# Kernel optimization log

Hardware: AMD Instinct MI355X
Metric: run time of the kernel (lower is better)

The kernel has to match this reference:

```python
import jax, jax.numpy as jnp
import numpy as np

IN_SIZE = 1024
HID = 2048
OUT = 1024
M_STEPS = 100   # max extra ponder steps -> up to M_STEPS+1 total steps
EPS = 0.01


def setup_inputs() -> dict:
    key = jax.random.key(0)
    ks = jax.random.split(key, 11)
    inv = 1.0 / np.sqrt(HID)

    def unif(k, shape, scale):
        return jax.random.uniform(k, shape, jnp.float32, -scale, scale)

    return {
        "x": jax.random.normal(ks[0], (IN_SIZE,), jnp.float32),
        "h0": jax.random.normal(ks[1], (HID,), jnp.float32) * 0.1,
        "c0": jax.random.normal(ks[2], (HID,), jnp.float32) * 0.1,
        "W_ih": unif(ks[3], (4 * HID, 1 + IN_SIZE), inv),
        "b_ih": unif(ks[4], (4 * HID,), inv),
        "W_hh": unif(ks[5], (4 * HID, HID), inv),
        "b_hh": unif(ks[6], (4 * HID,), inv),
        "w_halt": unif(ks[7], (HID,), inv),
        "b_halt": jnp.ones((1,), jnp.float32),  # fc_halt.bias = 1.0 per source
        "W_out": unif(ks[8], (OUT, HID), inv),
        "b_out": unif(ks[9], (OUT,), inv),
    }


def reference(x, h0, c0, W_ih, b_ih, W_hh, b_hh, w_halt, b_halt, W_out, b_out):
    # Input contribution is constant across steps except the prepended halt flag
    # (1 on first step, 0 after). Precompute it once.
    ih_x = W_ih[:, 1:] @ x + b_ih + b_hh      # (4H,)
    w_flag = W_ih[:, 0]                        # (4H,)

    def step(carry, flag):
        h, c = carry
        gates = ih_x + flag * w_flag + W_hh @ h  # (4H,)
        i, f, g, o = jnp.split(gates, 4)
        i = jax.nn.sigmoid(i)
        f = jax.nn.sigmoid(f)
        g = jnp.tanh(g)
        o = jax.nn.sigmoid(o)
        c = f * c + i * g
        h = o * jnp.tanh(c)
        return (h, c), (h, c)

    flags = jnp.concatenate(
        [jnp.ones((1,), x.dtype), jnp.zeros((M_STEPS,), x.dtype)])
    _, (H, C) = jax.lax.scan(step, (h0, c0), flags)  # (M+1, HID) each

    p = jax.nn.sigmoid(H @ w_halt + b_halt[0])       # (M+1,) halting probs
    csum = jnp.cumsum(p)
    halted = csum >= 1.0 - EPS
    # n = first step where cumulative halt prob crosses threshold, capped at M
    n = jnp.where(jnp.any(halted), jnp.argmax(halted), M_STEPS)
    # remainder r = 1 - sum(p[:n]); csum[n] - p[n] == sum(p[:n])
    r = 1.0 - jnp.where(n > 0, csum[n] - p[n], 0.0)

    idx = jnp.arange(M_STEPS + 1)
    w = jnp.where(idx < n, p, jnp.where(idx == n, r, 0.0))  # (M+1,)

    outputs = H @ W_out.T + b_out                    # (M+1, OUT)
    output = w @ outputs                             # (OUT,) weights sum to 1
    h_out = w @ H                                    # (HID,)
    c_out = w @ C                                    # (HID,)
    ponder = n.astype(x.dtype) + 1.0 + r
    return output, (h_out, c_out), ponder
```

## Files before the change

### kernel.cpp

```cpp
#include <hip/hip_runtime.h>


#define HID    2048
#define INS    1024
#define OUTS   1024
#define MSTEPS 100
#define NBLK   256
#define NTHR   512
#define NWAVE  8
#define JPB    8
#define RPB    32

typedef unsigned long long u64;

__device__ __forceinline__ float wave_reduce(float v) {
    #pragma unroll
    for (int off = 32; off > 0; off >>= 1)
        v += __shfl_down(v, off, 64);
    return v;
}

__device__ __forceinline__ u64 pack_tag(unsigned tag, float v) {
    return ((u64)tag << 32) | (u64)__float_as_uint(v);
}
__device__ __forceinline__ u64 aload(const u64* p) {
    return __hip_atomic_load(p, __ATOMIC_RELAXED, __HIP_MEMORY_SCOPE_AGENT);
}
__device__ __forceinline__ void astore(u64* p, u64 v) {
    __hip_atomic_store(p, v, __ATOMIC_RELAXED, __HIP_MEMORY_SCOPE_AGENT);
}


__global__ __launch_bounds__(NTHR) void alstm_kernel(
    const float* __restrict__ x,      const float* __restrict__ h0,
    const float* __restrict__ c0,     const float* __restrict__ W_ih,
    const float* __restrict__ b_ih,   const float* __restrict__ W_hh,
    const float* __restrict__ b_hh,   const float* __restrict__ w_halt,
    const float* __restrict__ b_halt, const float* __restrict__ W_out,
    const float* __restrict__ b_out,  float* __restrict__ out,
    float* __restrict__ ws)
{
    const int b    = blockIdx.x;
    const int tid  = threadIdx.x;
    const int wave = tid >> 6;
    const int lane = tid & 63;

    float* arrive = ws;
    float* mail   = ws + 1024;
    float* hbuf0  = ws + 2048;
    float* hbuf1  = ws + 2048 + HID;
    float* hbar_g = ws + 2048 + 2 * HID;

    __shared__ float h_lds[HID];
    __shared__ float x_lds[INS];
    __shared__ float gate_lds[RPB];
    __shared__ float ihx_lds[RPB];
    __shared__ float wflag_lds[RPB];
    __shared__ float red_lds[4];
    __shared__ float bcast_lds;
    __shared__ float psum[NWAVE];

    const float bh = b_halt[0];
    const int j_own = b * JPB + tid;

    const int lr0 = 4 * wave;

    #define SYNC_ROUND(tag_, part_, dot_) do {                                 \
        if (tid == 0) {                                                        \
            __threadfence();           \
            astore((u64*)(arrive + 4 * b), pack_tag((tag_), (part_)));         \
        }                                                                      \
        if (b == 0) {                                                          \
            float pf = 0.f;                                                    \
            if (tid < NBLK) {                                                  \
                u64 v;                                                         \
                do { v = aload((u64*)(arrive + 4 * tid)); }                    \
                while ((unsigned)(v >> 32) != (unsigned)(tag_));               \
                pf = __uint_as_float((unsigned)v);                             \
            }                                                                  \
            float s = wave_reduce(pf);                                         \
            if (lane == 0 && wave < 4) red_lds[wave] = s;                      \
            __syncthreads();                                                   \
            if (tid == 0)                                                      \
                bcast_lds = red_lds[0] + red_lds[1] + red_lds[2] + red_lds[3]; \
            __syncthreads();                                                   \
            if (tid < NBLK)                                                    \
                astore((u64*)(mail + 4 * tid), pack_tag((tag_), bcast_lds));   \
        }                                                                      \
        if (tid == 0) {                                                        \
            u64 v;                                                             \
            do { v = aload((u64*)(mail + 4 * b)); }                            \
            while ((unsigned)(v >> 32) != (unsigned)(tag_));                   \
            bcast_lds = __uint_as_float((unsigned)v);                          \
            __threadfence();        \
        }                                                                      \
        __syncthreads();                                                       \
        (dot_) = bcast_lds;                                                    \
    } while (0)

    ((float2*)x_lds)[tid] = ((const float2*)x)[tid];
    ((float4*)h_lds)[tid] = ((const float4*)h0)[tid];
    __syncthreads();

    #pragma unroll
    for (int rr = 0; rr < 4; ++rr) {
        const int lr = lr0 + rr;
        const int r  = (lr >> 3) * HID + b * JPB + (lr & 7);
        const float* wrow = W_ih + (size_t)r * (INS + 1) + 1;
        const int mis = (r + 1) & 3;
        const int p0  = (4 - mis) & 3;
        const int nv  = (INS - p0) >> 2;
        const float4* wv = (const float4*)(wrow + p0);
        float acc = 0.f;
        for (int i = lane; i < nv; i += 64) {
            float4 w4 = wv[i];
            int k = p0 + 4 * i;
            acc += w4.x * x_lds[k] + w4.y * x_lds[k + 1]
                 + w4.z * x_lds[k + 2] + w4.w * x_lds[k + 3];
        }
        if (lane == 0) {
            for (int k = 0; k < p0; ++k)            acc += wrow[k] * x_lds[k];
            for (int k = p0 + 4 * nv; k < INS; ++k) acc += wrow[k] * x_lds[k];
        }
        acc = wave_reduce(acc);
        if (lane == 0) {
            ihx_lds[lr]   = acc + b_ih[r] + b_hh[r];
            wflag_lds[lr] = W_ih[(size_t)r * (INS + 1)];
        }
    }

    float c_reg = 0.f, h_reg = 0.f, hbar = 0.f, cbar = 0.f;
    if (tid < JPB) c_reg = c0[j_own];

    const float4* wr0;
    const float4* wr1;
    const float4* wr2;
    const float4* wr3;
    {
        const int r = (lr0 >> 3) * HID + b * JPB + (lr0 & 7);
        wr0 = (const float4*)(W_hh + (size_t)r * HID);
        wr1 = (const float4*)(W_hh + (size_t)(r + 1) * HID);
        wr2 = (const float4*)(W_hh + (size_t)(r + 2) * HID);
        wr3 = (const float4*)(W_hh + (size_t)(r + 3) * HID);
    }

    float csum = 0.f, r_halt = 0.f;
    int   n_halt = 0;
    for (int t = 0; t <= MSTEPS; ++t) {
        {
            const float4* hv = (const float4*)h_lds;
            float a0 = 0.f, a1 = 0.f, a2 = 0.f, a3 = 0.f;
            #pragma unroll
            for (int m = 0; m < 8; ++m) {
                float4 hh = hv[lane + 64 * m];
                float4 w0 = wr0[lane + 64 * m];
                float4 w1 = wr1[lane + 64 * m];
                float4 w2 = wr2[lane + 64 * m];
                float4 w3 = wr3[lane + 64 * m];
                a0 += w0.x * hh.x + w0.y * hh.y + w0.z * hh.z + w0.w * hh.w;
                a1 += w1.x * hh.x + w1.y * hh.y + w1.z * hh.z + w1.w * hh.w;
                a2 += w2.x * hh.x + w2.y * hh.y + w2.z * hh.z + w2.w * hh.w;
                a3 += w3.x * hh.x + w3.y * hh.y + w3.z * hh.z + w3.w * hh.w;
            }
            a0 = wave_reduce(a0);
            a1 = wave_reduce(a1);
            a2 = wave_reduce(a2);
            a3 = wave_reduce(a3);
            if (lane == 0) {
                #pragma unroll
                for (int rr = 0; rr < 4; ++rr) {
                    float av = (rr == 0) ? a0 : (rr == 1) ? a1 : (rr == 2) ? a2 : a3;
                    float bb = ihx_lds[lr0 + rr];
                    if (t == 0) bb += wflag_lds[lr0 + rr];
                    gate_lds[lr0 + rr] = bb + av;
                }
            }
        }
        __syncthreads();

        float part = 0.f;
        float* hdst = (t & 1) ? hbuf1 : hbuf0;
        if (tid < JPB) {
            float iv = gate_lds[0 * JPB + tid];
            float fv = gate_lds[1 * JPB + tid];
            float gv = gate_lds[2 * JPB + tid];
            float ov = gate_lds[3 * JPB + tid];
            iv = 1.f / (1.f + expf(-iv));
            fv = 1.f / (1.f + expf(-fv));
            gv = tanhf(gv);
            ov = 1.f / (1.f + expf(-ov));
            c_reg = fv * c_reg + iv * gv;
            h_reg = ov * tanhf(c_reg);
            hdst[j_own] = h_reg;
            part = h_reg * w_halt[j_own];
        }
        part += __shfl_down(part, 4, 64);
        part += __shfl_down(part, 2, 64);
        part += __shfl_down(part, 1, 64);

        float dotv;
        SYNC_ROUND(t + 1, part, dotv);

        float p = 1.f / (1.f + expf(-(dotv + bh)));
        float prev = csum;
        csum += p;
        bool halt_now = (csum >= 1.f - 0.01f) || (t == MSTEPS);
        float wt = halt_now ? (1.f - prev) : p;
        if (tid < JPB) { hbar += wt * h_reg; cbar += wt * c_reg; }
        if (halt_now) { n_halt = t; r_halt = 1.f - prev; break; }

        __syncthreads();
        ((float4*)h_lds)[tid] = ((const float4*)hdst)[tid];
        __syncthreads();
    }

    if (tid < JPB) {
        out[OUTS + j_own]       = hbar;
        out[OUTS + HID + j_own] = cbar;
        hbar_g[j_own] = hbar;
    }
    if (b == 0 && tid == 0) out[OUTS + 2 * HID] = (float)(n_halt + 1) + r_halt;

    float dummy;
    SYNC_ROUND(n_halt + 2, 0.f, dummy);
    (void)dummy;

    __syncthreads();
    ((float4*)h_lds)[tid] = ((const float4*)hbar_g)[tid];
    __syncthreads();

    {
        const int row  = b * 4 + (wave & 3);
        const int half = wave >> 2;
        const float4* wrow = (const float4*)(W_out + (size_t)row * HID) + half * 256;
        const float4* hv   = (const float4*)h_lds + half * 256;
        float acc = 0.f;
        #pragma unroll
        for (int m = 0; m < 4; ++m) {
            float4 w4 = wrow[lane + 64 * m];
            float4 h4 = hv[lane + 64 * m];
            acc += w4.x * h4.x + w4.y * h4.y + w4.z * h4.z + w4.w * h4.w;
        }
        acc = wave_reduce(acc);
        if (lane == 0) psum[wave] = acc;
    }
    __syncthreads();
    if (tid < 4) {
        int row = b * 4 + tid;
        out[row] = psum[tid] + psum[tid + 4] + b_out[row];
    }
    #undef SYNC_ROUND
}

extern "C" void kernel_launch(void* const* d_in, const int* in_sizes, int n_in,
                              void* d_out, int out_size, void* d_ws, size_t ws_size,
                              hipStream_t stream) {
    const float* x      = (const float*)d_in[0];
    const float* h0     = (const float*)d_in[1];
    const float* c0     = (const float*)d_in[2];
    const float* W_ih   = (const float*)d_in[3];
    const float* b_ih   = (const float*)d_in[4];
    const float* W_hh   = (const float*)d_in[5];
    const float* b_hh   = (const float*)d_in[6];
    const float* w_halt = (const float*)d_in[7];
    const float* b_halt = (const float*)d_in[8];
    const float* W_out  = (const float*)d_in[9];
    const float* b_out  = (const float*)d_in[10];
    float* out = (float*)d_out;
    float* ws  = (float*)d_ws;

    hipMemsetAsync(d_ws, 0, 8192, stream);

    alstm_kernel<<<dim3(NBLK), dim3(NTHR), 0, stream>>>(
        x, h0, c0, W_ih, b_ih, W_hh, b_hh, w_halt, b_halt, W_out, b_out,
        out, ws);
}
```

Baseline: 187.6 us.

## Keep recurrent and output weight slices resident in registers across all steps

Each wave's four W_hh rows (32 float4 per lane) and its W_out slice (4 float4) are loaded once before the recurrence and held in VGPRs. Empty asm constraints stop the compiler from rematerialising them as reloads. This removes the per-step global/L2 reads of the 32 MB W_hh matrix over the 101 sequential steps. The cost is about 144 extra VGPRs per lane, which risks spilling or lower occupancy, though the persistent grid runs only one 512-thread block per CU.

Result: faster. 177.6 us (-5.3%).

```diff
diff --git a/kernel.cpp b/kernel.cpp
--- a/kernel.cpp
+++ b/kernel.cpp
@@ -12,6 +12,8 @@
 #define RPB    32
 
 typedef unsigned long long u64;
+
+#define KEEP4(v) asm volatile("" : "+v"((v).x), "+v"((v).y), "+v"((v).z), "+v"((v).w))
 
 __device__ __forceinline__ float wave_reduce(float v) {
     #pragma unroll
@@ -64,6 +66,7 @@
     const int j_own = b * JPB + tid;
 
     const int lr0 = 4 * wave;
+    const int rbase = (lr0 >> 3) * HID + b * JPB + (lr0 & 7);
 
     #define SYNC_ROUND(tag_, part_, dot_) do {                                 \
         if (tid == 0) {                                                        \
@@ -98,6 +101,29 @@
         (dot_) = bcast_lds;                                                    \
     } while (0)
 
+    float4 w0r[8], w1r[8], w2r[8], w3r[8];
+    {
+        const float4* p0 = (const float4*)(W_hh + (size_t)rbase * HID);
+        const float4* p1 = (const float4*)(W_hh + (size_t)(rbase + 1) * HID);
+        const float4* p2 = (const float4*)(W_hh + (size_t)(rbase + 2) * HID);
+        const float4* p3 = (const float4*)(W_hh + (size_t)(rbase + 3) * HID);
+        #pragma unroll
+        for (int m = 0; m < 8; ++m) {
+            w0r[m] = p0[lane + 64 * m];
+            w1r[m] = p1[lane + 64 * m];
+            w2r[m] = p2[lane + 64 * m];
+            w3r[m] = p3[lane + 64 * m];
+        }
+    }
+    const int orow  = b * 4 + (wave & 3);
+    const int ohalf = wave >> 2;
+    float4 wor[4];
+    {
+        const float4* po = (const float4*)(W_out + (size_t)orow * HID) + ohalf * 256;
+        #pragma unroll
+        for (int m = 0; m < 4; ++m) wor[m] = po[lane + 64 * m];
+    }
+
     ((float2*)x_lds)[tid] = ((const float2*)x)[tid];
     ((float4*)h_lds)[tid] = ((const float4*)h0)[tid];
     __syncthreads();
@@ -129,20 +155,15 @@
         }
     }
 
+    #pragma unroll
+    for (int m = 0; m < 8; ++m) {
+        KEEP4(w0r[m]); KEEP4(w1r[m]); KEEP4(w2r[m]); KEEP4(w3r[m]);
+    }
+    #pragma unroll
+    for (int m = 0; m < 4; ++m) KEEP4(wor[m]);
+
     float c_reg = 0.f, h_reg = 0.f, hbar = 0.f, cbar = 0.f;
     if (tid < JPB) c_reg = c0[j_own];
-
-    const float4* wr0;
-    const float4* wr1;
-    const float4* wr2;
-    const float4* wr3;
-    {
-        const int r = (lr0 >> 3) * HID + b * JPB + (lr0 & 7);
-        wr0 = (const float4*)(W_hh + (size_t)r * HID);
-        wr1 = (const float4*)(W_hh + (size_t)(r + 1) * HID);
-        wr2 = (const float4*)(W_hh + (size_t)(r + 2) * HID);
-        wr3 = (const float4*)(W_hh + (size_t)(r + 3) * HID);
-    }
 
     float csum = 0.f, r_halt = 0.f;
     int   n_halt = 0;
@@ -153,27 +174,26 @@
             #pragma unroll
             for (int m = 0; m < 8; ++m) {
                 float4 hh = hv[lane + 64 * m];
-                float4 w0 = wr0[lane + 64 * m];
-                float4 w1 = wr1[lane + 64 * m];
-                float4 w2 = wr2[lane + 64 * m];
-                float4 w3 = wr3[lane + 64 * m];
-                a0 += w0.x * hh.x + w0.y * hh.y + w0.z * hh.z + w0.w * hh.w;
-                a1 += w1.x * hh.x + w1.y * hh.y + w1.z * hh.z + w1.w * hh.w;
-                a2 += w2.x * hh.x + w2.y * hh.y + w2.z * hh.z + w2.w * hh.w;
-                a3 += w3.x * hh.x + w3.y * hh.y + w3.z * hh.z + w3.w * hh.w;
+                a0 += w0r[m].x * hh.x + w0r[m].y * hh.y + w0r[m].z * hh.z + w0r[m].w * hh.w;
+                a1 += w1r[m].x * hh.x + w1r[m].y * hh.y + w1r[m].z * hh.z + w1r[m].w * hh.w;
+                a2 += w2r[m].x * hh.x + w2r[m].y * hh.y + w2r[m].z * hh.z + w2r[m].w * hh.w;
+                a3 += w3r[m].x * hh.x + w3r[m].y * hh.y + w3r[m].z * hh.z + w3r[m].w * hh.w;
             }
             a0 = wave_reduce(a0);
             a1 = wave_reduce(a1);
             a2 = wave_reduce(a2);
             a3 = wave_reduce(a3);
             if (lane == 0) {
-                #pragma unroll
-                for (int rr = 0; rr < 4; ++rr) {
-                    float av = (rr == 0) ? a0 : (rr == 1) ? a1 : (rr == 2) ? a2 : a3;
-                    float bb = ihx_lds[lr0 + rr];
-                    if (t == 0) bb += wflag_lds[lr0 + rr];
-                    gate_lds[lr0 + rr] = bb + av;
+                float bb0 = ihx_lds[lr0 + 0], bb1 = ihx_lds[lr0 + 1];
+                float bb2 = ihx_lds[lr0 + 2], bb3 = ihx_lds[lr0 + 3];
+                if (t == 0) {
+                    bb0 += wflag_lds[lr0 + 0]; bb1 += wflag_lds[lr0 + 1];
+                    bb2 += wflag_lds[lr0 + 2]; bb3 += wflag_lds[lr0 + 3];
                 }
+                gate_lds[lr0 + 0] = bb0 + a0;
+                gate_lds[lr0 + 1] = bb1 + a1;
+                gate_lds[lr0 + 2] = bb2 + a2;
+                gate_lds[lr0 + 3] = bb3 + a3;
             }
         }
         __syncthreads();
@@ -230,16 +250,13 @@
     __syncthreads();
 
     {
-        const int row  = b * 4 + (wave & 3);
-        const int half = wave >> 2;
-        const float4* wrow = (const float4*)(W_out + (size_t)row * HID) + half * 256;
-        const float4* hv   = (const float4*)h_lds + half * 256;
+        const float4* hv = (const float4*)h_lds + ohalf * 256;
         float acc = 0.f;
         #pragma unroll
         for (int m = 0; m < 4; ++m) {
-            float4 w4 = wrow[lane + 64 * m];
             float4 h4 = hv[lane + 64 * m];
-            acc += w4.x * h4.x + w4.y * h4.y + w4.z * h4.z + w4.w * h4.w;
+            acc += wor[m].x * h4.x + wor[m].y * h4.y
+                 + wor[m].z * h4.z + wor[m].w * h4.w;
         }
         acc = wave_reduce(acc);
         if (lane == 0) psum[wave] = acc;
```

## Stream W_hh and W_ih rows through LDS via async global_load_lds double-buffering

Applied to the files above, without the earlier changes.

Each step's W_hh dot products now stage weight chunks into per-wave double-buffered LDS using global_load_lds DMA, with explicit vmcnt waits so the next load overlaps the current FMA work. The W_ih precompute uses the same staging to handle rows that are not 16-byte aligned. The h vector is now reloaded at the start of each step, which removes one barrier pair. Sync slots are padded to 64 bytes to avoid false sharing. This adds about 80KB of LDS and hand-tuned waitcnt logic, with a risk of ordering bugs.

Result: no change. 190.4 us (+1.5%).

```diff
diff --git a/kernel.cpp b/kernel.cpp
--- a/kernel.cpp
+++ b/kernel.cpp
@@ -10,13 +10,27 @@
 #define NWAVE  8
 #define JPB    8
 #define RPB    32
+#define SLOTF  16
+#define STGF   1280
+#define WIH_TOT 8396800ULL
 
 typedef unsigned long long u64;
-
-__device__ __forceinline__ float wave_reduce(float v) {
+typedef unsigned int u32;
+
+#define AS1 __attribute__((address_space(1)))
+#define AS3 __attribute__((address_space(3)))
+
+__device__ __forceinline__ void dma16(const float* g, float* l) {
+    __builtin_amdgcn_global_load_lds((AS1 float*)(uintptr_t)g,
+                                     (AS3 float*)(u32)(uintptr_t)l, 16, 0, 0);
+}
+#define WAITV(n)  asm volatile("s_waitcnt vmcnt(" #n ")" ::: "memory")
+#define WAITLGKM() asm volatile("s_waitcnt lgkmcnt(0)" ::: "memory")
+
+__device__ __forceinline__ float wave_allreduce(float v) {
     #pragma unroll
     for (int off = 32; off > 0; off >>= 1)
-        v += __shfl_down(v, off, 64);
+        v += __shfl_xor(v, off, 64);
     return v;
 }
 
@@ -46,13 +60,14 @@
     const int lane = tid & 63;
 
     float* arrive = ws;
-    float* mail   = ws + 1024;
-    float* hbuf0  = ws + 2048;
-    float* hbuf1  = ws + 2048 + HID;
-    float* hbar_g = ws + 2048 + 2 * HID;
-
-    __shared__ float h_lds[HID];
-    __shared__ float x_lds[INS];
+    float* mail   = ws + NBLK * SLOTF;
+    float* hbuf0  = ws + 2 * NBLK * SLOTF;
+    float* hbuf1  = hbuf0 + HID;
+    float* hbar_g = hbuf0 + 2 * HID;
+
+    __shared__ __align__(16) float stage[NWAVE][2][STGF];
+    __shared__ __align__(16) float x_lds[INS];
+    __shared__ __align__(16) float h_lds[HID];
     __shared__ float gate_lds[RPB];
     __shared__ float ihx_lds[RPB];
     __shared__ float wflag_lds[RPB];
@@ -63,118 +78,159 @@
     const float bh = b_halt[0];
     const int j_own = b * JPB + tid;
 
-    const int lr0 = 4 * wave;
+    const int lr0   = 4 * wave;
+    const int rbase = (lr0 >> 3) * HID + b * JPB + (lr0 & 7);
 
     #define SYNC_ROUND(tag_, part_, dot_) do {                                 \
         if (tid == 0) {                                                        \
-            __threadfence();           \
-            astore((u64*)(arrive + 4 * b), pack_tag((tag_), (part_)));         \
+            __threadfence();                                                   \
+            astore((u64*)(arrive + SLOTF * b), pack_tag((tag_), (part_)));     \
         }                                                                      \
         if (b == 0) {                                                          \
             float pf = 0.f;                                                    \
             if (tid < NBLK) {                                                  \
                 u64 v;                                                         \
-                do { v = aload((u64*)(arrive + 4 * tid)); }                    \
+                do { v = aload((u64*)(arrive + SLOTF * tid)); }                \
                 while ((unsigned)(v >> 32) != (unsigned)(tag_));               \
                 pf = __uint_as_float((unsigned)v);                             \
             }                                                                  \
-            float s = wave_reduce(pf);                                         \
+            float s = wave_allreduce(pf);                                      \
             if (lane == 0 && wave < 4) red_lds[wave] = s;                      \
             __syncthreads();                                                   \
             if (tid == 0)                                                      \
                 bcast_lds = red_lds[0] + red_lds[1] + red_lds[2] + red_lds[3]; \
             __syncthreads();                                                   \
             if (tid < NBLK)                                                    \
-                astore((u64*)(mail + 4 * tid), pack_tag((tag_), bcast_lds));   \
+                astore((u64*)(mail + SLOTF * tid), pack_tag((tag_), bcast_lds)); \
         }                                                                      \
         if (tid == 0) {                                                        \
             u64 v;                                                             \
-            do { v = aload((u64*)(mail + 4 * b)); }                            \
+            do { v = aload((u64*)(mail + SLOTF * b)); }                        \
             while ((unsigned)(v >> 32) != (unsigned)(tag_));                   \
             bcast_lds = __uint_as_float((unsigned)v);                          \
-            __threadfence();        \
+            __threadfence();                                                   \
         }                                                                      \
         __syncthreads();                                                       \
         (dot_) = bcast_lds;                                                    \
     } while (0)
 
     ((float2*)x_lds)[tid] = ((const float2*)x)[tid];
-    ((float4*)h_lds)[tid] = ((const float4*)h0)[tid];
-    __syncthreads();
-
-    #pragma unroll
-    for (int rr = 0; rr < 4; ++rr) {
-        const int lr = lr0 + rr;
+    float bsum = 0.f, wflg = 0.f;
+    if (lane < 4) {
+        const int lr = lr0 + lane;
         const int r  = (lr >> 3) * HID + b * JPB + (lr & 7);
-        const float* wrow = W_ih + (size_t)r * (INS + 1) + 1;
-        const int mis = (r + 1) & 3;
-        const int p0  = (4 - mis) & 3;
-        const int nv  = (INS - p0) >> 2;
-        const float4* wv = (const float4*)(wrow + p0);
-        float acc = 0.f;
-        for (int i = lane; i < nv; i += 64) {
-            float4 w4 = wv[i];
-            int k = p0 + 4 * i;
-            acc += w4.x * x_lds[k] + w4.y * x_lds[k + 1]
-                 + w4.z * x_lds[k + 2] + w4.w * x_lds[k + 3];
-        }
-        if (lane == 0) {
-            for (int k = 0; k < p0; ++k)            acc += wrow[k] * x_lds[k];
-            for (int k = p0 + 4 * nv; k < INS; ++k) acc += wrow[k] * x_lds[k];
-        }
-        acc = wave_reduce(acc);
-        if (lane == 0) {
-            ihx_lds[lr]   = acc + b_ih[r] + b_hh[r];
-            wflag_lds[lr] = W_ih[(size_t)r * (INS + 1)];
-        }
-    }
-
+        bsum = b_ih[r] + b_hh[r];
+        wflg = W_ih[(size_t)r * 1025];
+    }
     float c_reg = 0.f, h_reg = 0.f, hbar = 0.f, cbar = 0.f;
     if (tid < JPB) c_reg = c0[j_own];
-
-    const float4* wr0;
-    const float4* wr1;
-    const float4* wr2;
-    const float4* wr3;
+    __syncthreads();
+
     {
-        const int r = (lr0 >> 3) * HID + b * JPB + (lr0 & 7);
-        wr0 = (const float4*)(W_hh + (size_t)r * HID);
-        wr1 = (const float4*)(W_hh + (size_t)(r + 1) * HID);
-        wr2 = (const float4*)(W_hh + (size_t)(r + 2) * HID);
-        wr3 = (const float4*)(W_hh + (size_t)(r + 3) * HID);
+        size_t pp[4]; u32 dd[4]; const float* cov[4]; int oob[4];
+        #pragma unroll
+        for (int rr = 0; rr < 4; ++rr) {
+            const int lr = lr0 + rr;
+            const int r  = (lr >> 3) * HID + b * JPB + (lr & 7);
+            size_t p = (size_t)r * 1025 + 1;
+            size_t a = p & ~(size_t)3;
+            pp[rr] = p; dd[rr] = (u32)(p - a);
+            cov[rr] = W_ih + a;
+            oob[rr] = (a + STGF > WIH_TOT);
+        }
+        #define IH_ISSUE(rr_) do {                                             \
+            const float* ga = cov[rr_] + 4 * lane;                             \
+            float* lb = &stage[wave][(rr_) & 1][0];                            \
+            dma16(ga,        lb);                                              \
+            dma16(ga +  256, lb +  256);                                       \
+            dma16(ga +  512, lb +  512);                                       \
+            dma16(ga +  768, lb +  768);                                       \
+            dma16(oob[rr_] ? cov[rr_] + 4 * lane : ga + 1024, lb + 1024);      \
+        } while (0)
+        #define IH_CONS(rr_, accv_) do {                                       \
+            float* sbuf = &stage[wave][(rr_) & 1][0];                          \
+            const u32 d = dd[rr_];                                             \
+            if (oob[rr_] && lane < (int)d) {           \
+                int k = 1024 - (int)d + lane;                                  \
+                sbuf[d + k] = W_ih[pp[rr_] + k];                               \
+            }                                                                  \
+            float acc = 0.f;                                                   \
+            _Pragma("unroll")                                                  \
+            for (int m = 0; m < 4; ++m) {                                      \
+                int k4 = lane + 64 * m; int k = 4 * k4;                        \
+                float4 x4 = ((const float4*)x_lds)[k4];                        \
+                acc += sbuf[d + k]     * x4.x + sbuf[d + k + 1] * x4.y         \
+                     + sbuf[d + k + 2] * x4.z + sbuf[d + k + 3] * x4.w;        \
+            }                                                                  \
+            (accv_) = acc;                                                     \
+        } while (0)
+        float i0, i1, i2, i3;
+        IH_ISSUE(0); IH_ISSUE(1);
+        WAITV(5); IH_CONS(0, i0); WAITLGKM(); IH_ISSUE(2);
+        WAITV(5); IH_CONS(1, i1); WAITLGKM(); IH_ISSUE(3);
+        WAITV(5); IH_CONS(2, i2);
+        WAITV(0); IH_CONS(3, i3);
+        i0 = wave_allreduce(i0); i1 = wave_allreduce(i1);
+        i2 = wave_allreduce(i2); i3 = wave_allreduce(i3);
+        if (lane < 4) {
+            float mine = (lane == 0) ? i0 : (lane == 1) ? i1 : (lane == 2) ? i2 : i3;
+            ihx_lds[lr0 + lane]   = mine + bsum;
+            wflag_lds[lr0 + lane] = wflg;
+        }
+        #undef IH_ISSUE
+        #undef IH_CONS
     }
 
     float csum = 0.f, r_halt = 0.f;
     int   n_halt = 0;
     for (int t = 0; t <= MSTEPS; ++t) {
+        const float* hsrc = (t == 0) ? h0 : ((t & 1) ? hbuf0 : hbuf1);
+        ((float4*)h_lds)[tid] = ((const float4*)hsrc)[tid];
+        __syncthreads();
+
+        float a0 = 0.f, a1 = 0.f, a2 = 0.f, a3 = 0.f;
         {
-            const float4* hv = (const float4*)h_lds;
-            float a0 = 0.f, a1 = 0.f, a2 = 0.f, a3 = 0.f;
-            #pragma unroll
-            for (int m = 0; m < 8; ++m) {
-                float4 hh = hv[lane + 64 * m];
-                float4 w0 = wr0[lane + 64 * m];
-                float4 w1 = wr1[lane + 64 * m];
-                float4 w2 = wr2[lane + 64 * m];
-                float4 w3 = wr3[lane + 64 * m];
-                a0 += w0.x * hh.x + w0.y * hh.y + w0.z * hh.z + w0.w * hh.w;
-                a1 += w1.x * hh.x + w1.y * hh.y + w1.z * hh.z + w1.w * hh.w;
-                a2 += w2.x * hh.x + w2.y * hh.y + w2.z * hh.z + w2.w * hh.w;
-                a3 += w3.x * hh.x + w3.y * hh.y + w3.z * hh.z + w3.w * hh.w;
-            }
-            a0 = wave_reduce(a0);
-            a1 = wave_reduce(a1);
-            a2 = wave_reduce(a2);
-            a3 = wave_reduce(a3);
-            if (lane == 0) {
-                #pragma unroll
-                for (int rr = 0; rr < 4; ++rr) {
-                    float av = (rr == 0) ? a0 : (rr == 1) ? a1 : (rr == 2) ? a2 : a3;
-                    float bb = ihx_lds[lr0 + rr];
-                    if (t == 0) bb += wflag_lds[lr0 + rr];
-                    gate_lds[lr0 + rr] = bb + av;
-                }
-            }
+            #define HH_ISSUE(c_) do {                                          \
+                const float* g = W_hh + (size_t)(rbase + ((c_) >> 1)) * HID    \
+                               + ((c_) & 1) * 1024 + 4 * lane;                 \
+                float* lb = &stage[wave][(c_) & 1][0];                         \
+                dma16(g,       lb);       dma16(g + 256, lb + 256);            \
+                dma16(g + 512, lb + 512); dma16(g + 768, lb + 768);            \
+            } while (0)
+            #define HH_CONS(c_) do {                                           \
+                const float4* wb = (const float4*)&stage[wave][(c_) & 1][0];   \
+                const float4* hb = (const float4*)(h_lds + ((c_) & 1) * 1024); \
+                float s = 0.f;                                                 \
+                _Pragma("unroll")                                              \
+                for (int m = 0; m < 4; ++m) {                                  \
+                    float4 w4 = wb[lane + 64 * m];                             \
+                    float4 h4 = hb[lane + 64 * m];                             \
+                    s += w4.x*h4.x + w4.y*h4.y + w4.z*h4.z + w4.w*h4.w;        \
+                }                                                              \
+                if      (((c_) >> 1) == 0) a0 += s;                            \
+                else if (((c_) >> 1) == 1) a1 += s;                            \
+                else if (((c_) >> 1) == 2) a2 += s;                            \
+                else                       a3 += s;                            \
+            } while (0)
+            HH_ISSUE(0); HH_ISSUE(1);
+            WAITV(4); HH_CONS(0); WAITLGKM(); HH_ISSUE(2);
+            WAITV(4); HH_CONS(1); WAITLGKM(); HH_ISSUE(3);
+            WAITV(4); HH_CONS(2); WAITLGKM(); HH_ISSUE(4);
+            WAITV(4); HH_CONS(3); WAITLGKM(); HH_ISSUE(5);
+            WAITV(4); HH_CONS(4); WAITLGKM(); HH_ISSUE(6);
+            WAITV(4); HH_CONS(5); WAITLGKM(); HH_ISSUE(7);
+            WAITV(4); HH_CONS(6);
+            WAITV(0); HH_CONS(7);
+            #undef HH_ISSUE
+            #undef HH_CONS
+        }
+        a0 = wave_allreduce(a0); a1 = wave_allreduce(a1);
+        a2 = wave_allreduce(a2); a3 = wave_allreduce(a3);
+        if (lane < 4) {
+            float mine = (lane == 0) ? a0 : (lane == 1) ? a1 : (lane == 2) ? a2 : a3;
+            float bb = ihx_lds[lr0 + lane];
+            if (t == 0) bb += wflag_lds[lr0 + lane];
+            gate_lds[lr0 + lane] = bb + mine;
         }
         __syncthreads();
 
@@ -208,10 +264,6 @@
         float wt = halt_now ? (1.f - prev) : p;
         if (tid < JPB) { hbar += wt * h_reg; cbar += wt * c_reg; }
         if (halt_now) { n_halt = t; r_halt = 1.f - prev; break; }
-
-        __syncthreads();
-        ((float4*)h_lds)[tid] = ((const float4*)hdst)[tid];
-        __syncthreads();
     }
 
     if (tid < JPB) {
@@ -225,15 +277,15 @@
     SYNC_ROUND(n_halt + 2, 0.f, dummy);
     (void)dummy;
 
-    __syncthreads();
-    ((float4*)h_lds)[tid] = ((const float4*)hbar_g)[tid];
+    float* hbar_lds = &stage[0][0][0];
+    ((float4*)hbar_lds)[tid] = ((const float4*)hbar_g)[tid];
     __syncthreads();
 
     {
         const int row  = b * 4 + (wave & 3);
         const int half = wave >> 2;
         const float4* wrow = (const float4*)(W_out + (size_t)row * HID) + half * 256;
-        const float4* hv   = (const float4*)h_lds + half * 256;
+        const float4* hv   = (const float4*)hbar_lds + half * 256;
         float acc = 0.f;
         #pragma unroll
         for (int m = 0; m < 4; ++m) {
@@ -241,7 +293,7 @@
             float4 h4 = hv[lane + 64 * m];
             acc += w4.x * h4.x + w4.y * h4.y + w4.z * h4.z + w4.w * h4.w;
         }
-        acc = wave_reduce(acc);
+        acc = wave_allreduce(acc);
         if (lane == 0) psum[wave] = acc;
     }
     __syncthreads();
@@ -269,7 +321,7 @@
     float* out = (float*)d_out;
     float* ws  = (float*)d_ws;
 
-    hipMemsetAsync(d_ws, 0, 8192, stream);
+    hipMemsetAsync(d_ws, 0, 32768, stream);
 
     alstm_kernel<<<dim3(NBLK), dim3(NTHR), 0, stream>>>(
         x, h0, c0, W_ih, b_ih, W_hh, b_hh, w_halt, b_halt, W_out, b_out,
```
